# Kernel tuning notes

Measured on AMD Instinct MI355X. Metric: run time of the kernel, lower is better.

## Reference

```python
import jax, jax.numpy as jnp
import numpy as np

M = 200000          # active voxels
N_CAM = 6           # cameras
C_IMG = 96          # image feature channels (img_dim)
H_FEAT, W_FEAT = 32, 88
PTS_DIM = 128
ORI_H, ORI_W = 256, 704   # batch_dict['ori_shape'][0]
GZ, GY, GX = 32, 512, 448 # voxel grid bounds (z,y,x)
BN_EPS = 1e-5


def setup_inputs() -> dict:
    key = jax.random.key(0)
    ks = jax.random.split(key, 12)
    cz = jax.random.randint(ks[0], (M,), 0, GZ)
    cy = jax.random.randint(ks[1], (M,), 0, GY)
    cx = jax.random.randint(ks[2], (M,), 0, GX)
    voxel_coords = jnp.stack([jnp.zeros((M,), jnp.int32), cz.astype(jnp.int32), cy.astype(jnp.int32), cx.astype(jnp.int32)], axis=1)
    pts_features = jax.random.normal(ks[3], (M, PTS_DIM), jnp.float32)
    img_feats = jax.random.normal(ks[4], (N_CAM, C_IMG, H_FEAT, W_FEAT), jnp.float32)
    eye = jnp.eye(4, dtype=jnp.float32)
    lidar2image = eye[None, None] + 0.1 * jax.random.normal(ks[5], (1, N_CAM, 4, 4), jnp.float32)
    img_aug_matrix = eye[None, None] + 0.01 * jax.random.normal(ks[6], (1, N_CAM, 4, 4), jnp.float32)
    lidar_aug_matrix = eye[None] + 0.01 * jax.random.normal(ks[7], (1, 4, 4), jnp.float32)
    conv_w = 0.02 * jax.random.normal(ks[8], (27, PTS_DIM + C_IMG, PTS_DIM), jnp.float32)
    bn_gamma = jnp.ones((PTS_DIM,), jnp.float32)
    bn_beta = jnp.zeros((PTS_DIM,), jnp.float32)
    bn_mean = 0.1 * jax.random.normal(ks[9], (PTS_DIM,), jnp.float32)
    bn_var = 1.0 + jax.random.uniform(ks[10], (PTS_DIM,), jnp.float32)
    return dict(pts_features=pts_features, voxel_coords=voxel_coords, img_feats=img_feats,
                lidar2image=lidar2image, img_aug_matrix=img_aug_matrix, lidar_aug_matrix=lidar_aug_matrix,
                conv_w=conv_w, bn_gamma=bn_gamma, bn_beta=bn_beta, bn_mean=bn_mean, bn_var=bn_var)


def _bilinear_sample(img, gx, gy):
    # img [C,H,W]; gx,gy [M] normalized to [-1,1]; align_corners=True, zero padding
    C, H, W = img.shape
    x = (gx + 1.0) * 0.5 * (W - 1)
    y = (gy + 1.0) * 0.5 * (H - 1)
    x0 = jnp.floor(x); y0 = jnp.floor(y)
    x1 = x0 + 1.0; y1 = y0 + 1.0
    wx1 = x - x0; wx0 = 1.0 - wx1
    wy1 = y - y0; wy0 = 1.0 - wy1
    imgf = img.reshape(C, H * W)
    def corner(xi, yi, w):
        valid = (xi >= 0) & (xi <= W - 1) & (yi >= 0) & (yi <= H - 1)
        xi_c = jnp.clip(xi, 0, W - 1).astype(jnp.int32)
        yi_c = jnp.clip(yi, 0, H - 1).astype(jnp.int32)
        return imgf[:, yi_c * W + xi_c] * (w * valid.astype(w.dtype))[None, :]
    return (corner(x0, y0, wx0 * wy0) + corner(x1, y0, wx1 * wy0)
            + corner(x0, y1, wx0 * wy1) + corner(x1, y1, wx1 * wy1))


def _forward(pts_features, voxel_coords, img_feats, lidar2image, img_aug_matrix,
             lidar_aug_matrix, conv_w, bn_gamma, bn_beta, bn_mean, bn_var):
    # ---- img_point_sampling_v2 (batch_size == 1, eval mode: no random noise) ----
    coords = voxel_coords[:, 1:][:, ::-1].astype(jnp.float32)     # (z,y,x) -> (x,y,z), [M,3]
    p = coords - lidar_aug_matrix[0, :3, 3]
    p = jnp.linalg.inv(lidar_aug_matrix[0, :3, :3]) @ p.T          # [3,M]
    c = jnp.einsum('nij,jm->nim', lidar2image[0, :, :3, :3], p) + lidar2image[0, :, :3, 3][:, :, None]  # [N,3,M]
    z = jnp.clip(c[:, 2], 1e-5, 1e5)
    xy = c[:, :2] / z[:, None, :]
    vec = jnp.concatenate([xy, z[:, None, :]], axis=1)             # [N,3,M]
    c2 = jnp.einsum('nij,njm->nim', img_aug_matrix[0, :, :3, :3], vec) + img_aug_matrix[0, :, :3, 3][:, :, None]
    gx = (c2[:, 0] / ORI_W - 0.5) * 2.0                            # [N,M]
    gy = (c2[:, 1] / ORI_H - 0.5) * 2.0
    sampled = jax.vmap(_bilinear_sample)(img_feats, gx, gy).sum(0)  # [C_IMG, M]

    # ---- fuse + sparse 3x3x3 conv over active voxels + BN + ReLU ----
    fuse = jnp.concatenate([pts_features, sampled.T], axis=1)      # [M, 224]
    cz, cy, cx = voxel_coords[:, 1], voxel_coords[:, 2], voxel_coords[:, 3]
    grid = jnp.full((GZ, GY, GX), -1, jnp.int32).at[cz, cy, cx].set(jnp.arange(M, dtype=jnp.int32))
    out = jnp.zeros((M, PTS_DIM), fuse.dtype)
    k = 0
    for dz in (-1, 0, 1):
        for dy in (-1, 0, 1):
            for dx in (-1, 0, 1):
                nz, ny, nx = cz + dz, cy + dy, cx + dx
                valid = (nz >= 0) & (nz < GZ) & (ny >= 0) & (ny < GY) & (nx >= 0) & (nx < GX)
                nid = grid[jnp.clip(nz, 0, GZ - 1), jnp.clip(ny, 0, GY - 1), jnp.clip(nx, 0, GX - 1)]
                nid = jnp.where(valid, nid, -1)
                feat = jnp.where((nid >= 0)[:, None], fuse[jnp.clip(nid, 0)], 0.0)
                out = out + feat @ conv_w[k]
                k += 1
    xhat = (out - bn_mean) * jax.lax.rsqrt(bn_var + BN_EPS)
    return jax.nn.relu(xhat * bn_gamma + bn_beta)


def reference(pts_features, voxel_coords, img_feats, lidar2image, img_aug_matrix,
              lidar_aug_matrix, conv_w, bn_gamma, bn_beta, bn_mean, bn_var):
    return _forward(pts_features, voxel_coords, img_feats, lidar2image, img_aug_matrix,
                    lidar_aug_matrix, conv_w, bn_gamma, bn_beta, bn_mean, bn_var)
```

## Files before the change

### kernel.cpp

```cpp
#include <hip/hip_runtime.h>
#include <hip/hip_bf16.h>
#include <hip/hip_fp16.h>

#define MPTS 200000
#define NCAM 6
#define CIMG 96
#define HF 32
#define WF 88
#define PDIM 128
#define FDIM 224
#define FDIM_P 232
#define ORIH 256
#define ORIW 704
#define GZD 32
#define GYD 512
#define GXD 448
#define NCELLS (GZD*GYD*GXD)
#define PAIR_CAP 16384
#define BN_EPS 1e-5f
#define TROWS 64

#define OFF_GRID   0UL
#define OFF_IMGT   29360128UL
#define OFF_DESCM  35848192UL
#define OFF_WPACK  OFF_DESCM
#define OFF_DESCW  40648192UL
#define OFF_FUSE   50248192UL
#define OFF_CNT    139848192UL
#define OFF_PAIRS  139848320UL

#define BPTS (MPTS*8/256)
#define BIMG (MPTS*12/256)

typedef __attribute__((ext_vector_type(8))) short bf16x8;
typedef __attribute__((ext_vector_type(4))) float f32x4;

__device__ __forceinline__ unsigned short f32_to_bf16bits(float f) {
    __hip_bfloat16 h = __float2bfloat16(f);
    return *reinterpret_cast<unsigned short*>(&h);
}

__device__ __forceinline__ float bf16bits_to_f32(unsigned short u) {
    return __uint_as_float(((unsigned int)u) << 16);
}

__device__ __forceinline__ ushort4 cvt4(float4 v) {
    ushort4 o;
    o.x = f32_to_bf16bits(v.x); o.y = f32_to_bf16bits(v.y);
    o.z = f32_to_bf16bits(v.z); o.w = f32_to_bf16bits(v.w);
    return o;
}

__global__ __launch_bounds__(256) void k_transpose(const float* __restrict__ img,
                                                   unsigned short* __restrict__ imgt) {
    int tid = blockIdx.x * 256 + threadIdx.x;
    if (tid >= NCAM*CIMG*HF*WF) return;
    int c = tid % CIMG;
    int r = tid / CIMG;
    int x = r % WF;
    int r2 = r / WF;
    int y = r2 % HF;
    int cam = r2 / HF;
    imgt[tid] = f32_to_bf16bits(img[((cam*CIMG + c)*HF + y)*WF + x]);
}

__global__ __launch_bounds__(256) void k_proj(const int* __restrict__ vc,
                                              const float* __restrict__ l2i,
                                              const float* __restrict__ iaug,
                                              const float* __restrict__ laug,
                                              int* __restrict__ grid,
                                              unsigned int* __restrict__ meta,
                                              uint2* __restrict__ wts) {
    int i = blockIdx.x * 256 + threadIdx.x;
    if (i >= MPTS) return;
    int cz = vc[i*4+1], cy = vc[i*4+2], cx = vc[i*4+3];
    atomicMax(&grid[(cz*GYD + cy)*GXD + cx], i);
    float cxf = (float)cx, cyf = (float)cy, czf = (float)cz;
    float a00=laug[0],a01=laug[1],a02=laug[2];
    float a10=laug[4],a11=laug[5],a12=laug[6];
    float a20=laug[8],a21=laug[9],a22=laug[10];
    float t0=laug[3], t1=laug[7], t2=laug[11];
    float det = a00*(a11*a22-a12*a21) - a01*(a10*a22-a12*a20) + a02*(a10*a21-a11*a20);
    float id = 1.0f/det;
    float b00 =  (a11*a22-a12*a21)*id, b01 = -(a01*a22-a02*a21)*id, b02 =  (a01*a12-a02*a11)*id;
    float b10 = -(a10*a22-a12*a20)*id, b11 =  (a00*a22-a02*a20)*id, b12 = -(a00*a12-a02*a10)*id;
    float b20 =  (a10*a21-a11*a20)*id, b21 = -(a00*a21-a01*a20)*id, b22 =  (a00*a11-a01*a10)*id;
    float px = cxf-t0, py = cyf-t1, pz = czf-t2;
    float X = b00*px + b01*py + b02*pz;
    float Y = b10*px + b11*py + b12*pz;
    float Z = b20*px + b21*py + b22*pz;
    #pragma unroll
    for (int cam = 0; cam < NCAM; cam++) {
        const float* Lm = l2i + cam*16;
        float c0 = Lm[0]*X + Lm[1]*Y + Lm[2]*Z  + Lm[3];
        float c1 = Lm[4]*X + Lm[5]*Y + Lm[6]*Z  + Lm[7];
        float c2 = Lm[8]*X + Lm[9]*Y + Lm[10]*Z + Lm[11];
        float z  = fminf(fmaxf(c2, 1e-5f), 100000.0f);
        float vx = c0/z, vy = c1/z, vz = z;
        const float* Am = iaug + cam*16;
        float d0 = Am[0]*vx + Am[1]*vy + Am[2]*vz + Am[3];
        float d1 = Am[4]*vx + Am[5]*vy + Am[6]*vz + Am[7];
        float x = d0 * ((float)(WF-1)/(float)ORIW);
        float y = d1 * ((float)(HF-1)/(float)ORIH);
        bool act = (x > -1.0f) && (x < (float)WF) && (y > -1.0f) && (y < (float)HF);
        float x0f = floorf(x), y0f = floorf(y);
        int x0 = (int)x0f, y0 = (int)y0f;
        float wx1 = x - x0f, wy1 = y - y0f;
        float wx0 = 1.f - wx1, wy0 = 1.f - wy1;
        float ux0, ux1, uy0, uy1;
        if (x0 < 0)            { ux0 = wx1; ux1 = 0.f; }
        else if (x0 >= WF-1)   { ux0 = 0.f; ux1 = wx0; }
        else                   { ux0 = wx0; ux1 = wx1; }
        if (y0 < 0)            { uy0 = wy1; uy1 = 0.f; }
        else if (y0 >= HF-1)   { uy0 = 0.f; uy1 = wy0; }
        else                   { uy0 = wy0; uy1 = wy1; }
        int xb = min(max(x0, 0), WF-2);
        int yb = min(max(y0, 0), HF-2);
        unsigned int m = 0u;
        __half2 h01 = __floats2half2_rn(0.f, 0.f), h23 = h01;
        if (act) {
            m = 0x8000u | (unsigned int)(yb*WF + xb);
            h01 = __floats2half2_rn(ux0*uy0, ux1*uy0);
            h23 = __floats2half2_rn(ux0*uy1, ux1*uy1);
        }
        meta[i*6 + cam] = m;
        uint2 wv;
        wv.x = *reinterpret_cast<unsigned int*>(&h01);
        wv.y = *reinterpret_cast<unsigned int*>(&h23);
        wts[i*6 + cam] = wv;
    }
}

__global__ __launch_bounds__(256) void k_fuse_pts(const float4* __restrict__ pts4,
                                                  ushort4* __restrict__ fuse4) {
    int t = blockIdx.x*256 + threadIdx.x;
    int i = t >> 3, c = t & 7;
    float4 v0 = pts4[i*32 + c];
    float4 v1 = pts4[i*32 + c + 8];
    float4 v2 = pts4[i*32 + c + 16];
    float4 v3 = pts4[i*32 + c + 24];
    fuse4[i*56 + c]      = cvt4(v0);
    fuse4[i*56 + c + 8]  = cvt4(v1);
    fuse4[i*56 + c + 16] = cvt4(v2);
    fuse4[i*56 + c + 24] = cvt4(v3);
}

__global__ __launch_bounds__(256) void k_fuse_img(const uint4* __restrict__ imgt16,
                                                  const unsigned int* __restrict__ meta,
                                                  const uint2* __restrict__ wts,
                                                  uint4* __restrict__ fuse16o) {
    int t = blockIdx.x*256 + threadIdx.x;
    int i = t / 12, sg = t % 12;
    unsigned int m[NCAM]; uint2 w[NCAM];
    #pragma unroll
    for (int cam = 0; cam < NCAM; cam++) { m[cam] = meta[i*6+cam]; w[cam] = wts[i*6+cam]; }
    float acc[8] = {0.f,0.f,0.f,0.f,0.f,0.f,0.f,0.f};
    #pragma unroll
    for (int cam = 0; cam < NCAM; cam++) {
        if (m[cam] & 0x8000u) {
            int pix = (int)(m[cam] & 0x1FFFu);
            const uint4* base = imgt16 + (size_t)cam*(HF*WF*(CIMG/8)) + (size_t)pix*(CIMG/8) + sg;
            uint4 t00 = base[0];
            uint4 t01 = base[(CIMG/8)];
            uint4 t10 = base[WF*(CIMG/8)];
            uint4 t11 = base[(WF+1)*(CIMG/8)];
            float2 w01 = __half22float2(*reinterpret_cast<const __half2*>(&w[cam].x));
            float2 w23 = __half22float2(*reinterpret_cast<const __half2*>(&w[cam].y));
            const unsigned short* s00 = reinterpret_cast<const unsigned short*>(&t00);
            const unsigned short* s01 = reinterpret_cast<const unsigned short*>(&t01);
            const unsigned short* s10 = reinterpret_cast<const unsigned short*>(&t10);
            const unsigned short* s11 = reinterpret_cast<const unsigned short*>(&t11);
            #pragma unroll
            for (int ch = 0; ch < 8; ch++) {
                acc[ch] += bf16bits_to_f32(s00[ch])*w01.x + bf16bits_to_f32(s01[ch])*w01.y
                         + bf16bits_to_f32(s10[ch])*w23.x + bf16bits_to_f32(s11[ch])*w23.y;
            }
        }
    }
    unsigned int o0 = (unsigned int)f32_to_bf16bits(acc[0]) | ((unsigned int)f32_to_bf16bits(acc[1]) << 16);
    unsigned int o1 = (unsigned int)f32_to_bf16bits(acc[2]) | ((unsigned int)f32_to_bf16bits(acc[3]) << 16);
    unsigned int o2 = (unsigned int)f32_to_bf16bits(acc[4]) | ((unsigned int)f32_to_bf16bits(acc[5]) << 16);
    unsigned int o3 = (unsigned int)f32_to_bf16bits(acc[6]) | ((unsigned int)f32_to_bf16bits(acc[7]) << 16);
    fuse16o[(size_t)i*28 + 16 + sg] = make_uint4(o0, o1, o2, o3);
}

__global__ __launch_bounds__(256) void k_wpack(const float* __restrict__ conv,
                                               ushort4* __restrict__ wp) {
    int tid = blockIdx.x * 256 + threadIdx.x;
    if (tid >= 27*7*8*64) return;
    int lane = tid & 63;
    int nt   = (tid >> 6) & 7;
    int kk   = (tid >> 9) % 7;
    int k27  = tid / 3584;
    int n     = nt*16 + (lane & 15);
    int kbase = kk*32 + (lane >> 4)*8;
    const float* src = conv + ((size_t)k27*FDIM + kbase)*PDIM + n;
    ushort4 lo, hi;
    lo.x = f32_to_bf16bits(src[0*PDIM]);
    lo.y = f32_to_bf16bits(src[1*PDIM]);
    lo.z = f32_to_bf16bits(src[2*PDIM]);
    lo.w = f32_to_bf16bits(src[3*PDIM]);
    hi.x = f32_to_bf16bits(src[4*PDIM]);
    hi.y = f32_to_bf16bits(src[5*PDIM]);
    hi.z = f32_to_bf16bits(src[6*PDIM]);
    hi.w = f32_to_bf16bits(src[7*PDIM]);
    wp[tid*2]   = lo;
    wp[tid*2+1] = hi;
}

__global__ __launch_bounds__(256) void k_pairs(const int* __restrict__ vc,
                                               const int* __restrict__ grid,
                                               int* __restrict__ cnt,
                                               int2* __restrict__ pairs) {
    int i = blockIdx.x * 256 + threadIdx.x;
    bool act = (i < MPTS);
    int cz = 0, cy = 0, cx = 0;
    if (act) { cz = vc[i*4+1]; cy = vc[i*4+2]; cx = vc[i*4+3]; }
    __shared__ int s_wcnt[4][27];
    __shared__ int s_wbase[4][27];
    int wv = threadIdx.x >> 6, ln = threadIdx.x & 63;
    int nid[27];
    int rnk[27];
    #pragma unroll
    for (int k = 0; k < 27; k++) {
        if (k == 13) continue;
        int dz = k/9 - 1, dy = (k/3)%3 - 1, dx = k%3 - 1;
        int nz = cz+dz, ny = cy+dy, nx = cx+dx;
        int id = -1;
        if (act && nz >= 0 && nz < GZD && ny >= 0 && ny < GYD && nx >= 0 && nx < GXD)
            id = grid[(nz*GYD + ny)*GXD + nx];
        nid[k] = id;
        unsigned long long mm = __ballot(id >= 0);
        if (ln == 0) s_wcnt[wv][k] = __popcll(mm);
        rnk[k] = __popcll(mm & ((1ull << ln) - 1ull));
    }
    __syncthreads();
    if (threadIdx.x < 27 && threadIdx.x != 13) {
        int k = threadIdx.x;
        int c0 = s_wcnt[0][k], c1 = s_wcnt[1][k], c2 = s_wcnt[2][k], c3 = s_wcnt[3][k];
        int tot = c0 + c1 + c2 + c3;
        int bse = (tot > 0) ? atomicAdd(&cnt[k], tot) : 0;
        s_wbase[0][k] = bse;
        s_wbase[1][k] = bse + c0;
        s_wbase[2][k] = bse + c0 + c1;
        s_wbase[3][k] = bse + c0 + c1 + c2;
    }
    __syncthreads();
    #pragma unroll
    for (int k = 0; k < 27; k++) {
        if (k == 13) continue;
        if (nid[k] >= 0) {
            int slot = s_wbase[wv][k] + rnk[k];
            if (slot < PAIR_CAP) pairs[k*PAIR_CAP + slot] = make_int2(i, nid[k]);
        }
    }
}

__device__ __forceinline__ void fill_tile64(unsigned short (*s_fb)[FDIM_P],
                                            const int* s_j,
                                            const uint4* __restrict__ fuse16,
                                            int tid) {
    #pragma unroll
    for (int it = 0; it < (TROWS*28)/256; it++) {
        int idx = it*256 + tid;
        int r = idx / 28, c = idx % 28;
        int j = s_j[r];
        uint4 v = make_uint4(0u, 0u, 0u, 0u);
        if (j >= 0) v = fuse16[(size_t)j*28 + c];
        *reinterpret_cast<uint4*>(&s_fb[r][c*8]) = v;
    }
}

__device__ __forceinline__ void gemm_mfma64(const unsigned short (*s_fb)[FDIM_P],
                                            const bf16x8* __restrict__ wpb,
                                            int k27, int lane, int wv,
                                            f32x4 acc[4][2]) {
    int quad = lane >> 4, l15 = lane & 15;
    bf16x8 b[7][2];
    #pragma unroll
    for (int kk = 0; kk < 7; kk++) {
        b[kk][0] = wpb[(((k27*7 + kk)*8) + wv*2 + 0)*64 + lane];
        b[kk][1] = wpb[(((k27*7 + kk)*8) + wv*2 + 1)*64 + lane];
    }
    #pragma unroll
    for (int kk = 0; kk < 7; kk++) {
        #pragma unroll
        for (int mt = 0; mt < 4; mt++) {
            bf16x8 a = *reinterpret_cast<const bf16x8*>(&s_fb[mt*16 + l15][kk*32 + quad*8]);
            acc[mt][0] = __builtin_amdgcn_mfma_f32_16x16x32_bf16(a, b[kk][0], acc[mt][0], 0, 0, 0);
            acc[mt][1] = __builtin_amdgcn_mfma_f32_16x16x32_bf16(a, b[kk][1], acc[mt][1], 0, 0, 0);
        }
    }
}

__global__ __launch_bounds__(256) void k_nbr(const int2* __restrict__ pairs,
                                             const int* __restrict__ cnt,
                                             const uint4* __restrict__ fuse16,
                                             const bf16x8* __restrict__ wpb,
                                             float* __restrict__ out) {
    int k = blockIdx.y;
    if (k >= 13) k += 1;
    int n = cnt[k];
    if (n > PAIR_CAP) n = PAIR_CAP;
    int p0 = blockIdx.x * TROWS;
    if (p0 >= n) return;
    int nn = min(TROWS, n - p0);

    __shared__ int s_i[TROWS];
    __shared__ int s_j[TROWS];
    __shared__ unsigned short s_fb[TROWS][FDIM_P];
    int tid = threadIdx.x;
    if (tid < TROWS) {
        if (tid < nn) { int2 pr = pairs[k*PAIR_CAP + p0 + tid]; s_i[tid] = pr.x; s_j[tid] = pr.y; }
        else          { s_i[tid] = -1; s_j[tid] = -1; }
    }
    __syncthreads();
    fill_tile64(s_fb, s_j, fuse16, tid);
    __syncthreads();

    int lane = tid & 63, wv = tid >> 6;
    int quad = lane >> 4, l15 = lane & 15;
    f32x4 acc[4][2] = {};
    gemm_mfma64(s_fb, wpb, k, lane, wv, acc);

    #pragma unroll
    for (int nt = 0; nt < 2; nt++) {
        int col = wv*32 + nt*16 + l15;
        #pragma unroll
        for (int mt = 0; mt < 4; mt++) {
            #pragma unroll
            for (int r = 0; r < 4; r++) {
                int row = mt*16 + quad*4 + r;
                int ii = s_i[row];
                if (ii >= 0) unsafeAtomicAdd(&out[(size_t)ii*PDIM + col], acc[mt][nt][r]);
            }
        }
    }
}

__global__ __launch_bounds__(256) void k_center(const int* __restrict__ vc,
                                                const int* __restrict__ grid,
                                                const uint4* __restrict__ fuse16,
                                                const bf16x8* __restrict__ wpb,
                                                const float* __restrict__ gamma,
                                                const float* __restrict__ beta,
                                                const float* __restrict__ mean,
                                                const float* __restrict__ var,
                                                float* __restrict__ out) {
    int i0 = blockIdx.x * TROWS;
    __shared__ int s_j[TROWS];
    __shared__ unsigned short s_fb[TROWS][FDIM_P];
    int tid = threadIdx.x;
    if (tid < TROWS) {
        int i = i0 + tid;
        int cz = vc[i*4+1], cy = vc[i*4+2], cx = vc[i*4+3];
        s_j[tid] = grid[(cz*GYD + cy)*GXD + cx];
    }
    __syncthreads();
    fill_tile64(s_fb, s_j, fuse16, tid);
    __syncthreads();

    int lane = tid & 63, wv = tid >> 6;
    int quad = lane >> 4, l15 = lane & 15;
    f32x4 acc[4][2] = {};
    gemm_mfma64(s_fb, wpb, 13, lane, wv, acc);

    #pragma unroll
    for (int nt = 0; nt < 2; nt++) {
        int col = wv*32 + nt*16 + l15;
        float g  = gamma[col], bb = beta[col], mn = mean[col];
        float rs = rsqrtf(var[col] + BN_EPS);
        #pragma unroll
        for (int mt = 0; mt < 4; mt++) {
            #pragma unroll
            for (int r = 0; r < 4; r++) {
                int row = mt*16 + quad*4 + r;
                size_t o = (size_t)(i0 + row)*PDIM + col;
                float v = out[o] + acc[mt][nt][r];
                v = (v - mn)*rs*g + bb;
                out[o] = fmaxf(v, 0.f);
            }
        }
    }
}

extern "C" void kernel_launch(void* const* d_in, const int* in_sizes, int n_in,
                              void* d_out, int out_size, void* d_ws, size_t ws_size,
                              hipStream_t stream) {
    const float* pts   = (const float*)d_in[0];
    const int*   vc    = (const int*)d_in[1];
    const float* img   = (const float*)d_in[2];
    const float* l2i   = (const float*)d_in[3];
    const float* iaug  = (const float*)d_in[4];
    const float* laug  = (const float*)d_in[5];
    const float* conv  = (const float*)d_in[6];
    const float* gamma = (const float*)d_in[7];
    const float* beta  = (const float*)d_in[8];
    const float* mean  = (const float*)d_in[9];
    const float* var   = (const float*)d_in[10];
    float* out = (float*)d_out;

    char* ws = (char*)d_ws;
    int*            grid  = (int*)(ws + OFF_GRID);
    unsigned short* imgt  = (unsigned short*)(ws + OFF_IMGT);
    unsigned int*   descm = (unsigned int*)(ws + OFF_DESCM);
    uint2*          descw = (uint2*)(ws + OFF_DESCW);
    ushort4*        wp    = (ushort4*)(ws + OFF_WPACK);
    ushort4*        fuse4 = (ushort4*)(ws + OFF_FUSE);
    int*            cnt   = (int*)(ws + OFF_CNT);
    int2*           pairs = (int2*)(ws + OFF_PAIRS);
    const uint4*    fuse16 = (const uint4*)fuse4;
    uint4*          fuse16o = (uint4*)fuse4;
    const bf16x8*   wpb    = (const bf16x8*)wp;

    hipMemsetAsync(grid, 0xFF, (size_t)NCELLS*4, stream);
    hipMemsetAsync(cnt, 0, 32*4, stream);
    hipMemsetAsync(d_out, 0, (size_t)out_size*4, stream);

    int blocksM = (MPTS + 255)/256;
    k_transpose<<<(NCAM*CIMG*HF*WF + 255)/256, 256, 0, stream>>>(img, imgt);
    k_proj<<<blocksM, 256, 0, stream>>>(vc, l2i, iaug, laug, grid, descm, descw);
    k_fuse_pts<<<BPTS, 256, 0, stream>>>((const float4*)pts, fuse4);
    k_fuse_img<<<BIMG, 256, 0, stream>>>((const uint4*)imgt, descm, descw, fuse16o);
    k_wpack<<<(27*7*8*64 + 255)/256, 256, 0, stream>>>(conv, wp);
    k_pairs<<<blocksM, 256, 0, stream>>>(vc, grid, cnt, pairs);
    k_nbr<<<dim3(PAIR_CAP/TROWS, 26), 256, 0, stream>>>(pairs, cnt, fuse16, wpb, out);
    k_center<<<MPTS/TROWS, 256, 0, stream>>>(vc, grid, fuse16, wpb,
                                             gamma, beta, mean, var, out);
}
```

Baseline: 488.1 us.

## Fuse sparse conv into one output-stationary kernel with per-offset tile skipping

Replaces the pair-list build, the atomic scatter kernel over neighbor pairs and the separate center kernel with a single output-stationary kernel. Each block looks up all 27 neighbor ids for its 64 voxels, builds a per-offset mask of 16-row groups that have any neighbor, and gathers and runs MFMA only on those groups while keeping accumulators in registers. BN and ReLU are applied directly without a read-modify-write of the output. This drops the output memset, the pair buffers, the counter atomics and the float atomics, and removes the PAIR_CAP truncation. In exchange each block now loops over 27 offsets with two barriers per offset and issues grid lookups for every offset, even though most offsets are empty for this sparse data.

```diff
diff --git a/kernel.cpp b/kernel.cpp
--- a/kernel.cpp
+++ b/kernel.cpp
@@ -16,7 +16,6 @@
 #define GYD 512
 #define GXD 448
 #define NCELLS (GZD*GYD*GXD)
-#define PAIR_CAP 16384
 #define BN_EPS 1e-5f
 #define TROWS 64
 
@@ -26,8 +25,6 @@
 #define OFF_WPACK  OFF_DESCM
 #define OFF_DESCW  40648192UL
 #define OFF_FUSE   50248192UL
-#define OFF_CNT    139848192UL
-#define OFF_PAIRS  139848320UL
 
 #define BPTS (MPTS*8/256)
 #define BIMG (MPTS*12/256)
@@ -208,162 +205,95 @@
     wp[tid*2+1] = hi;
 }
 
-__global__ __launch_bounds__(256) void k_pairs(const int* __restrict__ vc,
-                                               const int* __restrict__ grid,
-                                               int* __restrict__ cnt,
-                                               int2* __restrict__ pairs) {
-    int i = blockIdx.x * 256 + threadIdx.x;
-    bool act = (i < MPTS);
-    int cz = 0, cy = 0, cx = 0;
-    if (act) { cz = vc[i*4+1]; cy = vc[i*4+2]; cx = vc[i*4+3]; }
-    __shared__ int s_wcnt[4][27];
-    __shared__ int s_wbase[4][27];
-    int wv = threadIdx.x >> 6, ln = threadIdx.x & 63;
-    int nid[27];
-    int rnk[27];
-    #pragma unroll
+__global__ __launch_bounds__(256) void k_conv(const int4* __restrict__ vc4,
+                                              const int* __restrict__ grid,
+                                              const uint4* __restrict__ fuse16,
+                                              const bf16x8* __restrict__ wpb,
+                                              const float* __restrict__ gamma,
+                                              const float* __restrict__ beta,
+                                              const float* __restrict__ mean,
+                                              const float* __restrict__ var,
+                                              float* __restrict__ out) {
+    int i0 = blockIdx.x * TROWS;
+    int tid = threadIdx.x;
+
+    __shared__ int s_cz[TROWS], s_cy[TROWS], s_cx[TROWS];
+    __shared__ int s_j[27][TROWS];
+    __shared__ unsigned int s_mask[27];
+    __shared__ unsigned short s_fb[TROWS][FDIM_P];
+
+    if (tid < TROWS) {
+        int4 v = vc4[i0 + tid];
+        s_cz[tid] = v.y; s_cy[tid] = v.z; s_cx[tid] = v.w;
+    }
+    __syncthreads();
+
+    for (int idx = tid; idx < 27*TROWS; idx += 256) {
+        int k = idx >> 6, r = idx & 63;
+        int dz = k/9 - 1, dy = (k/3)%3 - 1, dx = k%3 - 1;
+        int nz = s_cz[r]+dz, ny = s_cy[r]+dy, nx = s_cx[r]+dx;
+        int id = -1;
+        if (nz >= 0 && nz < GZD && ny >= 0 && ny < GYD && nx >= 0 && nx < GXD)
+            id = grid[(nz*GYD + ny)*GXD + nx];
+        s_j[k][r] = id;
+    }
+    __syncthreads();
+    if (tid < 27) {
+        unsigned int m = 0;
+        #pragma unroll 8
+        for (int r = 0; r < TROWS; r++)
+            if (s_j[tid][r] >= 0) m |= 1u << (r >> 4);
+        s_mask[tid] = m;
+    }
+    __syncthreads();
+
+    int lane = tid & 63, wv = tid >> 6;
+    int quad = lane >> 4, l15 = lane & 15;
+    int fr[7], fc[7];
+    #pragma unroll
+    for (int it = 0; it < 7; it++) {
+        int idx = it*256 + tid;
+        fr[it] = idx / 28; fc[it] = idx % 28;
+    }
+
+    f32x4 acc[4][2] = {};
+
     for (int k = 0; k < 27; k++) {
-        if (k == 13) continue;
-        int dz = k/9 - 1, dy = (k/3)%3 - 1, dx = k%3 - 1;
-        int nz = cz+dz, ny = cy+dy, nx = cx+dx;
-        int id = -1;
-        if (act && nz >= 0 && nz < GZD && ny >= 0 && ny < GYD && nx >= 0 && nx < GXD)
-            id = grid[(nz*GYD + ny)*GXD + nx];
-        nid[k] = id;
-        unsigned long long mm = __ballot(id >= 0);
-        if (ln == 0) s_wcnt[wv][k] = __popcll(mm);
-        rnk[k] = __popcll(mm & ((1ull << ln) - 1ull));
-    }
-    __syncthreads();
-    if (threadIdx.x < 27 && threadIdx.x != 13) {
-        int k = threadIdx.x;
-        int c0 = s_wcnt[0][k], c1 = s_wcnt[1][k], c2 = s_wcnt[2][k], c3 = s_wcnt[3][k];
-        int tot = c0 + c1 + c2 + c3;
-        int bse = (tot > 0) ? atomicAdd(&cnt[k], tot) : 0;
-        s_wbase[0][k] = bse;
-        s_wbase[1][k] = bse + c0;
-        s_wbase[2][k] = bse + c0 + c1;
-        s_wbase[3][k] = bse + c0 + c1 + c2;
-    }
-    __syncthreads();
-    #pragma unroll
-    for (int k = 0; k < 27; k++) {
-        if (k == 13) continue;
-        if (nid[k] >= 0) {
-            int slot = s_wbase[wv][k] + rnk[k];
-            if (slot < PAIR_CAP) pairs[k*PAIR_CAP + slot] = make_int2(i, nid[k]);
-        }
-    }
-}
-
-__device__ __forceinline__ void fill_tile64(unsigned short (*s_fb)[FDIM_P],
-                                            const int* s_j,
-                                            const uint4* __restrict__ fuse16,
-                                            int tid) {
-    #pragma unroll
-    for (int it = 0; it < (TROWS*28)/256; it++) {
-        int idx = it*256 + tid;
-        int r = idx / 28, c = idx % 28;
-        int j = s_j[r];
-        uint4 v = make_uint4(0u, 0u, 0u, 0u);
-        if (j >= 0) v = fuse16[(size_t)j*28 + c];
-        *reinterpret_cast<uint4*>(&s_fb[r][c*8]) = v;
-    }
-}
-
-__device__ __forceinline__ void gemm_mfma64(const unsigned short (*s_fb)[FDIM_P],
-                                            const bf16x8* __restrict__ wpb,
-                                            int k27, int lane, int wv,
-                                            f32x4 acc[4][2]) {
-    int quad = lane >> 4, l15 = lane & 15;
-    bf16x8 b[7][2];
-    #pragma unroll
-    for (int kk = 0; kk < 7; kk++) {
-        b[kk][0] = wpb[(((k27*7 + kk)*8) + wv*2 + 0)*64 + lane];
-        b[kk][1] = wpb[(((k27*7 + kk)*8) + wv*2 + 1)*64 + lane];
-    }
-    #pragma unroll
-    for (int kk = 0; kk < 7; kk++) {
+        unsigned int msk = s_mask[k];
+        if (msk == 0) continue;
+
+        bf16x8 b[7][2];
+        #pragma unroll
+        for (int kk = 0; kk < 7; kk++) {
+            b[kk][0] = wpb[(((k*7 + kk)*8) + wv*2 + 0)*64 + lane];
+            b[kk][1] = wpb[(((k*7 + kk)*8) + wv*2 + 1)*64 + lane];
+        }
+
+        #pragma unroll
+        for (int it = 0; it < 7; it++) {
+            int r = fr[it], c = fc[it];
+            if ((msk >> (r >> 4)) & 1u) {
+                int j = s_j[k][r];
+                uint4 v = make_uint4(0u, 0u, 0u, 0u);
+                if (j >= 0) v = fuse16[(size_t)j*28 + c];
+                *reinterpret_cast<uint4*>(&s_fb[r][c*8]) = v;
+            }
+        }
+        __syncthreads();
+
         #pragma unroll
         for (int mt = 0; mt < 4; mt++) {
-            bf16x8 a = *reinterpret_cast<const bf16x8*>(&s_fb[mt*16 + l15][kk*32 + quad*8]);
-            acc[mt][0] = __builtin_amdgcn_mfma_f32_16x16x32_bf16(a, b[kk][0], acc[mt][0], 0, 0, 0);
-            acc[mt][1] = __builtin_amdgcn_mfma_f32_16x16x32_bf16(a, b[kk][1], acc[mt][1], 0, 0, 0);
-        }
-    }
-}
-
-__global__ __launch_bounds__(256) void k_nbr(const int2* __restrict__ pairs,
-                                             const int* __restrict__ cnt,
-                                             const uint4* __restrict__ fuse16,
-                                             const bf16x8* __restrict__ wpb,
-                                             float* __restrict__ out) {
-    int k = blockIdx.y;
-    if (k >= 13) k += 1;
-    int n = cnt[k];
-    if (n > PAIR_CAP) n = PAIR_CAP;
-    int p0 = blockIdx.x * TROWS;
-    if (p0 >= n) return;
-    int nn = min(TROWS, n - p0);
-
-    __shared__ int s_i[TROWS];
-    __shared__ int s_j[TROWS];
-    __shared__ unsigned short s_fb[TROWS][FDIM_P];
-    int tid = threadIdx.x;
-    if (tid < TROWS) {
-        if (tid < nn) { int2 pr = pairs[k*PAIR_CAP + p0 + tid]; s_i[tid] = pr.x; s_j[tid] = pr.y; }
-        else          { s_i[tid] = -1; s_j[tid] = -1; }
-    }
-    __syncthreads();
-    fill_tile64(s_fb, s_j, fuse16, tid);
-    __syncthreads();
-
-    int lane = tid & 63, wv = tid >> 6;
-    int quad = lane >> 4, l15 = lane & 15;
-    f32x4 acc[4][2] = {};
-    gemm_mfma64(s_fb, wpb, k, lane, wv, acc);
-
-    #pragma unroll
-    for (int nt = 0; nt < 2; nt++) {
-        int col = wv*32 + nt*16 + l15;
-        #pragma unroll
-        for (int mt = 0; mt < 4; mt++) {
-            #pragma unroll
-            for (int r = 0; r < 4; r++) {
-                int row = mt*16 + quad*4 + r;
-                int ii = s_i[row];
-                if (ii >= 0) unsafeAtomicAdd(&out[(size_t)ii*PDIM + col], acc[mt][nt][r]);
+            if ((msk >> mt) & 1u) {
+                #pragma unroll
+                for (int kk = 0; kk < 7; kk++) {
+                    bf16x8 a = *reinterpret_cast<const bf16x8*>(&s_fb[mt*16 + l15][kk*32 + quad*8]);
+                    acc[mt][0] = __builtin_amdgcn_mfma_f32_16x16x32_bf16(a, b[kk][0], acc[mt][0], 0, 0, 0);
+                    acc[mt][1] = __builtin_amdgcn_mfma_f32_16x16x32_bf16(a, b[kk][1], acc[mt][1], 0, 0, 0);
+                }
             }
         }
-    }
-}
-
-__global__ __launch_bounds__(256) void k_center(const int* __restrict__ vc,
-                                                const int* __restrict__ grid,
-                                                const uint4* __restrict__ fuse16,
-                                                const bf16x8* __restrict__ wpb,
-                                                const float* __restrict__ gamma,
-                                                const float* __restrict__ beta,
-                                                const float* __restrict__ mean,
-                                                const float* __restrict__ var,
-                                                float* __restrict__ out) {
-    int i0 = blockIdx.x * TROWS;
-    __shared__ int s_j[TROWS];
-    __shared__ unsigned short s_fb[TROWS][FDIM_P];
-    int tid = threadIdx.x;
-    if (tid < TROWS) {
-        int i = i0 + tid;
-        int cz = vc[i*4+1], cy = vc[i*4+2], cx = vc[i*4+3];
-        s_j[tid] = grid[(cz*GYD + cy)*GXD + cx];
-    }
-    __syncthreads();
-    fill_tile64(s_fb, s_j, fuse16, tid);
-    __syncthreads();
-
-    int lane = tid & 63, wv = tid >> 6;
-    int quad = lane >> 4, l15 = lane & 15;
-    f32x4 acc[4][2] = {};
-    gemm_mfma64(s_fb, wpb, 13, lane, wv, acc);
+        __syncthreads();
+    }
 
     #pragma unroll
     for (int nt = 0; nt < 2; nt++) {
@@ -375,10 +305,9 @@
             #pragma unroll
             for (int r = 0; r < 4; r++) {
                 int row = mt*16 + quad*4 + r;
-                size_t o = (size_t)(i0 + row)*PDIM + col;
-                float v = out[o] + acc[mt][nt][r];
+                float v = acc[mt][nt][r];
                 v = (v - mn)*rs*g + bb;
-                out[o] = fmaxf(v, 0.f);
+                out[(size_t)(i0 + row)*PDIM + col] = fmaxf(v, 0.f);
             }
         }
     }
@@ -407,15 +336,11 @@
     uint2*          descw = (uint2*)(ws + OFF_DESCW);
     ushort4*        wp    = (ushort4*)(ws + OFF_WPACK);
     ushort4*        fuse4 = (ushort4*)(ws + OFF_FUSE);
-    int*            cnt   = (int*)(ws + OFF_CNT);
-    int2*           pairs = (int2*)(ws + OFF_PAIRS);
     const uint4*    fuse16 = (const uint4*)fuse4;
     uint4*          fuse16o = (uint4*)fuse4;
     const bf16x8*   wpb    = (const bf16x8*)wp;
 
     hipMemsetAsync(grid, 0xFF, (size_t)NCELLS*4, stream);
-    hipMemsetAsync(cnt, 0, 32*4, stream);
-    hipMemsetAsync(d_out, 0, (size_t)out_size*4, stream);
 
     int blocksM = (MPTS + 255)/256;
     k_transpose<<<(NCAM*CIMG*HF*WF + 255)/256, 256, 0, stream>>>(img, imgt);
@@ -423,8 +348,6 @@
     k_fuse_pts<<<BPTS, 256, 0, stream>>>((const float4*)pts, fuse4);
     k_fuse_img<<<BIMG, 256, 0, stream>>>((const uint4*)imgt, descm, descw, fuse16o);
     k_wpack<<<(27*7*8*64 + 255)/256, 256, 0, stream>>>(conv, wp);
-    k_pairs<<<blocksM, 256, 0, stream>>>(vc, grid, cnt, pairs);
-    k_nbr<<<dim3(PAIR_CAP/TROWS, 26), 256, 0, stream>>>(pairs, cnt, fuse16, wpb, out);
-    k_center<<<MPTS/TROWS, 256, 0, stream>>>(vc, grid, fuse16, wpb,
-                                             gamma, beta, mean, var, out);
-}
+    k_conv<<<MPTS/TROWS, 256, 0, stream>>>((const int4*)vc, grid, fuse16, wpb,
+                                           gamma, beta, mean, var, out);
+}
```

Result: slower. 521.9 us (+6.9%).

## Merge memsets and independent prep kernels into fused block-partitioned launches

Applied to the files above, without the earlier changes.

Replaces three hipMemsetAsync calls and the transpose, weight-pack and point-feature conversion kernels with one k_prep kernel whose block ranges each do one job. The image sampling and neighbour-pair building kernels are merged into one k_samp launch in the same way. The workspace layout is compacted so the weight pack no longer aliases the descriptor buffer. This cuts launch count and inter-kernel gaps and lets independent work run at the same time, at the cost of mixed-workload blocks in one grid.

```diff
diff --git a/kernel.cpp b/kernel.cpp
--- a/kernel.cpp
+++ b/kernel.cpp
@@ -22,15 +22,29 @@
 
 #define OFF_GRID   0UL
 #define OFF_IMGT   29360128UL
-#define OFF_DESCM  35848192UL
-#define OFF_WPACK  OFF_DESCM
-#define OFF_DESCW  40648192UL
-#define OFF_FUSE   50248192UL
-#define OFF_CNT    139848192UL
-#define OFF_PAIRS  139848320UL
-
-#define BPTS (MPTS*8/256)
-#define BIMG (MPTS*12/256)
+#define OFF_DESCM  32604160UL
+#define OFF_DESCW  37404160UL
+#define OFF_WPACK  47004160UL
+#define OFF_FUSE   48552448UL
+#define OFF_CNT    138152448UL
+#define OFF_PAIRS  138152576UL
+
+#define B_GRIDCLR 1792
+#define B_OUTCLR  6250
+#define B_CNTCLR  1
+#define B_TRANS   6336
+#define B_WPACK   378
+#define B_FPTS    6250
+#define P0 (B_GRIDCLR)
+#define P1 (P0 + B_OUTCLR)
+#define P2 (P1 + B_CNTCLR)
+#define P3 (P2 + B_TRANS)
+#define P4 (P3 + B_WPACK)
+#define B_PREP (P4 + B_FPTS)
+
+#define B_FIMG  9375
+#define B_PAIRS 782
+#define B_SAMP (B_FIMG + B_PAIRS)
 
 typedef __attribute__((ext_vector_type(8))) short bf16x8;
 typedef __attribute__((ext_vector_type(4))) float f32x4;
@@ -51,17 +65,68 @@
     return o;
 }
 
-__global__ __launch_bounds__(256) void k_transpose(const float* __restrict__ img,
-                                                   unsigned short* __restrict__ imgt) {
-    int tid = blockIdx.x * 256 + threadIdx.x;
-    if (tid >= NCAM*CIMG*HF*WF) return;
-    int c = tid % CIMG;
-    int r = tid / CIMG;
-    int x = r % WF;
-    int r2 = r / WF;
-    int y = r2 % HF;
-    int cam = r2 / HF;
-    imgt[tid] = f32_to_bf16bits(img[((cam*CIMG + c)*HF + y)*WF + x]);
+__global__ __launch_bounds__(256) void k_prep(const float* __restrict__ img,
+                                              unsigned short* __restrict__ imgt,
+                                              const float* __restrict__ conv,
+                                              ushort4* __restrict__ wp,
+                                              const float4* __restrict__ pts4,
+                                              ushort4* __restrict__ fuse4,
+                                              uint4* __restrict__ grid4,
+                                              float4* __restrict__ out4,
+                                              int* __restrict__ cnt) {
+    int b = blockIdx.x, tid = threadIdx.x;
+    if (b < P0) {
+        uint4 v = make_uint4(~0u, ~0u, ~0u, ~0u);
+        uint4* p = grid4 + (size_t)(b*256 + tid)*4;
+        p[0] = v; p[1] = v; p[2] = v; p[3] = v;
+    } else if (b < P1) {
+        int t = (b - P0)*256 + tid;
+        float4 z = make_float4(0.f, 0.f, 0.f, 0.f);
+        float4* p = out4 + (size_t)t*4;
+        p[0] = z; p[1] = z; p[2] = z; p[3] = z;
+    } else if (b < P2) {
+        if (tid < 32) cnt[tid] = 0;
+    } else if (b < P3) {
+        int t = (b - P2)*256 + tid;
+        int c = t % CIMG;
+        int r = t / CIMG;
+        int x = r % WF;
+        int r2 = r / WF;
+        int y = r2 % HF;
+        int cam = r2 / HF;
+        imgt[t] = f32_to_bf16bits(img[((cam*CIMG + c)*HF + y)*WF + x]);
+    } else if (b < P4) {
+        int t = (b - P3)*256 + tid;
+        int lane = t & 63;
+        int nt   = (t >> 6) & 7;
+        int kk   = (t >> 9) % 7;
+        int k27  = t / 3584;
+        int n     = nt*16 + (lane & 15);
+        int kbase = kk*32 + (lane >> 4)*8;
+        const float* src = conv + ((size_t)k27*FDIM + kbase)*PDIM + n;
+        ushort4 lo, hi;
+        lo.x = f32_to_bf16bits(src[0*PDIM]);
+        lo.y = f32_to_bf16bits(src[1*PDIM]);
+        lo.z = f32_to_bf16bits(src[2*PDIM]);
+        lo.w = f32_to_bf16bits(src[3*PDIM]);
+        hi.x = f32_to_bf16bits(src[4*PDIM]);
+        hi.y = f32_to_bf16bits(src[5*PDIM]);
+        hi.z = f32_to_bf16bits(src[6*PDIM]);
+        hi.w = f32_to_bf16bits(src[7*PDIM]);
+        wp[t*2]   = lo;
+        wp[t*2+1] = hi;
+    } else {
+        int t = (b - P4)*256 + tid;
+        int i = t >> 3, c = t & 7;
+        float4 v0 = pts4[i*32 + c];
+        float4 v1 = pts4[i*32 + c + 8];
+        float4 v2 = pts4[i*32 + c + 16];
+        float4 v3 = pts4[i*32 + c + 24];
+        fuse4[i*56 + c]      = cvt4(v0);
+        fuse4[i*56 + c + 8]  = cvt4(v1);
+        fuse4[i*56 + c + 16] = cvt4(v2);
+        fuse4[i*56 + c + 24] = cvt4(v3);
+    }
 }
 
 __global__ __launch_bounds__(256) void k_proj(const int* __restrict__ vc,
@@ -131,127 +196,91 @@
     }
 }
 
-__global__ __launch_bounds__(256) void k_fuse_pts(const float4* __restrict__ pts4,
-                                                  ushort4* __restrict__ fuse4) {
-    int t = blockIdx.x*256 + threadIdx.x;
-    int i = t >> 3, c = t & 7;
-    float4 v0 = pts4[i*32 + c];
-    float4 v1 = pts4[i*32 + c + 8];
-    float4 v2 = pts4[i*32 + c + 16];
-    float4 v3 = pts4[i*32 + c + 24];
-    fuse4[i*56 + c]      = cvt4(v0);
-    fuse4[i*56 + c + 8]  = cvt4(v1);
-    fuse4[i*56 + c + 16] = cvt4(v2);
-    fuse4[i*56 + c + 24] = cvt4(v3);
-}
-
-__global__ __launch_bounds__(256) void k_fuse_img(const uint4* __restrict__ imgt16,
-                                                  const unsigned int* __restrict__ meta,
-                                                  const uint2* __restrict__ wts,
-                                                  uint4* __restrict__ fuse16o) {
-    int t = blockIdx.x*256 + threadIdx.x;
-    int i = t / 12, sg = t % 12;
-    unsigned int m[NCAM]; uint2 w[NCAM];
-    #pragma unroll
-    for (int cam = 0; cam < NCAM; cam++) { m[cam] = meta[i*6+cam]; w[cam] = wts[i*6+cam]; }
-    float acc[8] = {0.f,0.f,0.f,0.f,0.f,0.f,0.f,0.f};
-    #pragma unroll
-    for (int cam = 0; cam < NCAM; cam++) {
-        if (m[cam] & 0x8000u) {
-            int pix = (int)(m[cam] & 0x1FFFu);
-            const uint4* base = imgt16 + (size_t)cam*(HF*WF*(CIMG/8)) + (size_t)pix*(CIMG/8) + sg;
-            uint4 t00 = base[0];
-            uint4 t01 = base[(CIMG/8)];
-            uint4 t10 = base[WF*(CIMG/8)];
-            uint4 t11 = base[(WF+1)*(CIMG/8)];
-            float2 w01 = __half22float2(*reinterpret_cast<const __half2*>(&w[cam].x));
-            float2 w23 = __half22float2(*reinterpret_cast<const __half2*>(&w[cam].y));
-            const unsigned short* s00 = reinterpret_cast<const unsigned short*>(&t00);
-            const unsigned short* s01 = reinterpret_cast<const unsigned short*>(&t01);
-            const unsigned short* s10 = reinterpret_cast<const unsigned short*>(&t10);
-            const unsigned short* s11 = reinterpret_cast<const unsigned short*>(&t11);
-            #pragma unroll
-            for (int ch = 0; ch < 8; ch++) {
-                acc[ch] += bf16bits_to_f32(s00[ch])*w01.x + bf16bits_to_f32(s01[ch])*w01.y
-                         + bf16bits_to_f32(s10[ch])*w23.x + bf16bits_to_f32(s11[ch])*w23.y;
-            }
-        }
-    }
-    unsigned int o0 = (unsigned int)f32_to_bf16bits(acc[0]) | ((unsigned int)f32_to_bf16bits(acc[1]) << 16);
-    unsigned int o1 = (unsigned int)f32_to_bf16bits(acc[2]) | ((unsigned int)f32_to_bf16bits(acc[3]) << 16);
-    unsigned int o2 = (unsigned int)f32_to_bf16bits(acc[4]) | ((unsigned int)f32_to_bf16bits(acc[5]) << 16);
-    unsigned int o3 = (unsigned int)f32_to_bf16bits(acc[6]) | ((unsigned int)f32_to_bf16bits(acc[7]) << 16);
-    fuse16o[(size_t)i*28 + 16 + sg] = make_uint4(o0, o1, o2, o3);
-}
-
-__global__ __launch_bounds__(256) void k_wpack(const float* __restrict__ conv,
-                                               ushort4* __restrict__ wp) {
-    int tid = blockIdx.x * 256 + threadIdx.x;
-    if (tid >= 27*7*8*64) return;
-    int lane = tid & 63;
-    int nt   = (tid >> 6) & 7;
-    int kk   = (tid >> 9) % 7;
-    int k27  = tid / 3584;
-    int n     = nt*16 + (lane & 15);
-    int kbase = kk*32 + (lane >> 4)*8;
-    const float* src = conv + ((size_t)k27*FDIM + kbase)*PDIM + n;
-    ushort4 lo, hi;
-    lo.x = f32_to_bf16bits(src[0*PDIM]);
-    lo.y = f32_to_bf16bits(src[1*PDIM]);
-    lo.z = f32_to_bf16bits(src[2*PDIM]);
-    lo.w = f32_to_bf16bits(src[3*PDIM]);
-    hi.x = f32_to_bf16bits(src[4*PDIM]);
-    hi.y = f32_to_bf16bits(src[5*PDIM]);
-    hi.z = f32_to_bf16bits(src[6*PDIM]);
-    hi.w = f32_to_bf16bits(src[7*PDIM]);
-    wp[tid*2]   = lo;
-    wp[tid*2+1] = hi;
-}
-
-__global__ __launch_bounds__(256) void k_pairs(const int* __restrict__ vc,
-                                               const int* __restrict__ grid,
-                                               int* __restrict__ cnt,
-                                               int2* __restrict__ pairs) {
-    int i = blockIdx.x * 256 + threadIdx.x;
-    bool act = (i < MPTS);
-    int cz = 0, cy = 0, cx = 0;
-    if (act) { cz = vc[i*4+1]; cy = vc[i*4+2]; cx = vc[i*4+3]; }
+__global__ __launch_bounds__(256) void k_samp(const uint4* __restrict__ imgt16,
+                                              const unsigned int* __restrict__ meta,
+                                              const uint2* __restrict__ wts,
+                                              uint4* __restrict__ fuse16o,
+                                              const int* __restrict__ vc,
+                                              const int* __restrict__ grid,
+                                              int* __restrict__ cnt,
+                                              int2* __restrict__ pairs) {
     __shared__ int s_wcnt[4][27];
     __shared__ int s_wbase[4][27];
-    int wv = threadIdx.x >> 6, ln = threadIdx.x & 63;
-    int nid[27];
-    int rnk[27];
-    #pragma unroll
-    for (int k = 0; k < 27; k++) {
-        if (k == 13) continue;
-        int dz = k/9 - 1, dy = (k/3)%3 - 1, dx = k%3 - 1;
-        int nz = cz+dz, ny = cy+dy, nx = cx+dx;
-        int id = -1;
-        if (act && nz >= 0 && nz < GZD && ny >= 0 && ny < GYD && nx >= 0 && nx < GXD)
-            id = grid[(nz*GYD + ny)*GXD + nx];
-        nid[k] = id;
-        unsigned long long mm = __ballot(id >= 0);
-        if (ln == 0) s_wcnt[wv][k] = __popcll(mm);
-        rnk[k] = __popcll(mm & ((1ull << ln) - 1ull));
-    }
-    __syncthreads();
-    if (threadIdx.x < 27 && threadIdx.x != 13) {
-        int k = threadIdx.x;
-        int c0 = s_wcnt[0][k], c1 = s_wcnt[1][k], c2 = s_wcnt[2][k], c3 = s_wcnt[3][k];
-        int tot = c0 + c1 + c2 + c3;
-        int bse = (tot > 0) ? atomicAdd(&cnt[k], tot) : 0;
-        s_wbase[0][k] = bse;
-        s_wbase[1][k] = bse + c0;
-        s_wbase[2][k] = bse + c0 + c1;
-        s_wbase[3][k] = bse + c0 + c1 + c2;
-    }
-    __syncthreads();
-    #pragma unroll
-    for (int k = 0; k < 27; k++) {
-        if (k == 13) continue;
-        if (nid[k] >= 0) {
-            int slot = s_wbase[wv][k] + rnk[k];
-            if (slot < PAIR_CAP) pairs[k*PAIR_CAP + slot] = make_int2(i, nid[k]);
+    int b = blockIdx.x, tid = threadIdx.x;
+    if (b < B_FIMG) {
+        int t = b*256 + tid;
+        int i = t / 12, sg = t % 12;
+        unsigned int m[NCAM]; uint2 w[NCAM];
+        #pragma unroll
+        for (int cam = 0; cam < NCAM; cam++) { m[cam] = meta[i*6+cam]; w[cam] = wts[i*6+cam]; }
+        float acc[8] = {0.f,0.f,0.f,0.f,0.f,0.f,0.f,0.f};
+        #pragma unroll
+        for (int cam = 0; cam < NCAM; cam++) {
+            if (m[cam] & 0x8000u) {
+                int pix = (int)(m[cam] & 0x1FFFu);
+                const uint4* base = imgt16 + (size_t)cam*(HF*WF*(CIMG/8)) + (size_t)pix*(CIMG/8) + sg;
+                uint4 t00 = base[0];
+                uint4 t01 = base[(CIMG/8)];
+                uint4 t10 = base[WF*(CIMG/8)];
+                uint4 t11 = base[(WF+1)*(CIMG/8)];
+                float2 w01 = __half22float2(*reinterpret_cast<const __half2*>(&w[cam].x));
+                float2 w23 = __half22float2(*reinterpret_cast<const __half2*>(&w[cam].y));
+                const unsigned short* s00 = reinterpret_cast<const unsigned short*>(&t00);
+                const unsigned short* s01 = reinterpret_cast<const unsigned short*>(&t01);
+                const unsigned short* s10 = reinterpret_cast<const unsigned short*>(&t10);
+                const unsigned short* s11 = reinterpret_cast<const unsigned short*>(&t11);
+                #pragma unroll
+                for (int ch = 0; ch < 8; ch++) {
+                    acc[ch] += bf16bits_to_f32(s00[ch])*w01.x + bf16bits_to_f32(s01[ch])*w01.y
+                             + bf16bits_to_f32(s10[ch])*w23.x + bf16bits_to_f32(s11[ch])*w23.y;
+                }
+            }
+        }
+        unsigned int o0 = (unsigned int)f32_to_bf16bits(acc[0]) | ((unsigned int)f32_to_bf16bits(acc[1]) << 16);
+        unsigned int o1 = (unsigned int)f32_to_bf16bits(acc[2]) | ((unsigned int)f32_to_bf16bits(acc[3]) << 16);
+        unsigned int o2 = (unsigned int)f32_to_bf16bits(acc[4]) | ((unsigned int)f32_to_bf16bits(acc[5]) << 16);
+        unsigned int o3 = (unsigned int)f32_to_bf16bits(acc[6]) | ((unsigned int)f32_to_bf16bits(acc[7]) << 16);
+        fuse16o[(size_t)i*28 + 16 + sg] = make_uint4(o0, o1, o2, o3);
+    } else {
+        int i = (b - B_FIMG)*256 + tid;
+        bool act = (i < MPTS);
+        int cz = 0, cy = 0, cx = 0;
+        if (act) { cz = vc[i*4+1]; cy = vc[i*4+2]; cx = vc[i*4+3]; }
+        int wv = tid >> 6, ln = tid & 63;
+        int nid[27];
+        int rnk[27];
+        #pragma unroll
+        for (int k = 0; k < 27; k++) {
+            if (k == 13) continue;
+            int dz = k/9 - 1, dy = (k/3)%3 - 1, dx = k%3 - 1;
+            int nz = cz+dz, ny = cy+dy, nx = cx+dx;
+            int id = -1;
+            if (act && nz >= 0 && nz < GZD && ny >= 0 && ny < GYD && nx >= 0 && nx < GXD)
+                id = grid[(nz*GYD + ny)*GXD + nx];
+            nid[k] = id;
+            unsigned long long mm = __ballot(id >= 0);
+            if (ln == 0) s_wcnt[wv][k] = __popcll(mm);
+            rnk[k] = __popcll(mm & ((1ull << ln) - 1ull));
+        }
+        __syncthreads();
+        if (tid < 27 && tid != 13) {
+            int k = tid;
+            int c0 = s_wcnt[0][k], c1 = s_wcnt[1][k], c2 = s_wcnt[2][k], c3 = s_wcnt[3][k];
+            int tot = c0 + c1 + c2 + c3;
+            int bse = (tot > 0) ? atomicAdd(&cnt[k], tot) : 0;
+            s_wbase[0][k] = bse;
+            s_wbase[1][k] = bse + c0;
+            s_wbase[2][k] = bse + c0 + c1;
+            s_wbase[3][k] = bse + c0 + c1 + c2;
+        }
+        __syncthreads();
+        #pragma unroll
+        for (int k = 0; k < 27; k++) {
+            if (k == 13) continue;
+            if (nid[k] >= 0) {
+                int slot = s_wbase[wv][k] + rnk[k];
+                if (slot < PAIR_CAP) pairs[k*PAIR_CAP + slot] = make_int2(i, nid[k]);
+            }
         }
     }
 }
@@ -413,17 +442,11 @@
     uint4*          fuse16o = (uint4*)fuse4;
     const bf16x8*   wpb    = (const bf16x8*)wp;
 
-    hipMemsetAsync(grid, 0xFF, (size_t)NCELLS*4, stream);
-    hipMemsetAsync(cnt, 0, 32*4, stream);
-    hipMemsetAsync(d_out, 0, (size_t)out_size*4, stream);
-
-    int blocksM = (MPTS + 255)/256;
-    k_transpose<<<(NCAM*CIMG*HF*WF + 255)/256, 256, 0, stream>>>(img, imgt);
-    k_proj<<<blocksM, 256, 0, stream>>>(vc, l2i, iaug, laug, grid, descm, descw);
-    k_fuse_pts<<<BPTS, 256, 0, stream>>>((const float4*)pts, fuse4);
-    k_fuse_img<<<BIMG, 256, 0, stream>>>((const uint4*)imgt, descm, descw, fuse16o);
-    k_wpack<<<(27*7*8*64 + 255)/256, 256, 0, stream>>>(conv, wp);
-    k_pairs<<<blocksM, 256, 0, stream>>>(vc, grid, cnt, pairs);
+    k_prep<<<B_PREP, 256, 0, stream>>>(img, imgt, conv, wp, (const float4*)pts,
+                                       fuse4, (uint4*)grid, (float4*)out, cnt);
+    k_proj<<<(MPTS + 255)/256, 256, 0, stream>>>(vc, l2i, iaug, laug, grid, descm, descw);
+    k_samp<<<B_SAMP, 256, 0, stream>>>((const uint4*)imgt, descm, descw, fuse16o,
+                                       vc, grid, cnt, pairs);
     k_nbr<<<dim3(PAIR_CAP/TROWS, 26), 256, 0, stream>>>(pairs, cnt, fuse16, wpb, out);
     k_center<<<MPTS/TROWS, 256, 0, stream>>>(vc, grid, fuse16, wpb,
                                              gamma, beta, mean, var, out);
```

New measurement: 492.9 us. No clear change (+1.0%).
